# Optimization experiments

Measured on AMD Instinct MI355X. Metric: run time of the kernel, lower is better.

The kernel has to match this reference:

```python
import jax, jax.numpy as jnp
import numpy as np

NUM_CAPS_OUT = 10
NUM_NODES = 32 * 6 * 6  # 1152
IN_DIM = 8
OUT_DIM = 16
ROUTING_ITERS = 3


def squash(x):
    # scale = |x|^2/(1+|x|^2); out = scale * x/|x|  (no epsilon, faithful to torch)
    sn = jnp.sum(x * x, axis=-1, keepdims=True)
    return sn / (1.0 + sn) * x / jnp.sqrt(sn)


def setup_inputs() -> dict:
    key = jax.random.key(0)
    ks = jax.random.split(key, 6)
    B = 512
    images = jax.random.normal(ks[0], (B, 1, 28, 28), dtype=jnp.float32)
    # ConvLayer: Conv2d(1, 256, k=9, s=1) with bias
    conv1_w = jax.random.normal(ks[1], (256, 1, 9, 9), dtype=jnp.float32) * 0.05
    conv1_b = jnp.zeros((256,), dtype=jnp.float32)
    prim_w = jax.random.normal(ks[2], (8 * 32, 256, 9, 9), dtype=jnp.float32) * 0.01
    prim_b = jnp.zeros((8 * 32,), dtype=jnp.float32)
    # DigitCaps weight: torch.randn(10, 1152, 8, 16)
    W = jax.random.normal(ks[3], (NUM_CAPS_OUT, NUM_NODES, IN_DIM, OUT_DIM), dtype=jnp.float32)
    return {"images": images, "conv1_w": conv1_w, "conv1_b": conv1_b,
            "prim_w": prim_w, "prim_b": prim_b, "W": W}


def reference(images, conv1_w, conv1_b, prim_w, prim_b, W):
    B = images.shape[0]
    dn = ('NCHW', 'OIHW', 'NCHW')
    # ConvLayer: 28x28 -> 20x20, 256 channels, ReLU
    x = jax.lax.conv_general_dilated(images, conv1_w, (1, 1), 'VALID', dimension_numbers=dn)
    x = jax.nn.relu(x + conv1_b[None, :, None, None])  # [B,256,20,20]
    # PrimaryCaps: 8 stacked convs -> [B, 8*32, 6, 6]; each capsule viewed as (32*6*6,)
    u = jax.lax.conv_general_dilated(x, prim_w, (2, 2), 'VALID', dimension_numbers=dn)
    u = u + prim_b[None, :, None, None]
    u = u.reshape(B, 8, NUM_NODES).transpose(0, 2, 1)  # [B,1152,8]
    u = squash(u)
    # DigitCaps: u_hat[c,b,n,o] = sum_i u[b,n,i] * W[c,n,i,o]
    u_hat = jnp.einsum('bni,cnio->cbno', u, W)  # [10,B,1152,16]
    # Dynamic routing (3 iterations). b_ij kept as [...,1]: torch replicates it
    # across the 16 out dims identically, so math is unchanged.
    b_ij = jnp.zeros(u_hat.shape[:-1] + (1,), dtype=u_hat.dtype)
    v_j = None
    for it in range(ROUTING_ITERS):
        c_ij = jax.nn.softmax(b_ij, axis=2)            # softmax over nodes
        s_j = jnp.sum(c_ij * u_hat, axis=2, keepdims=True)  # [10,B,1,16]
        v_j = squash(s_j)
        if it < ROUTING_ITERS - 1:
            a_ij = jnp.sum(u_hat * v_j, axis=-1, keepdims=True)  # [10,B,1152,1]
            b_ij = b_ij + a_ij
    # squeeze -> [10,B,16], transpose(0,1) -> [B,10,16]
    return v_j[:, :, 0, :].transpose(1, 0, 2)
```

## Files before the change

### kernel.cpp

```cpp
#include <hip/hip_runtime.h>
#include <hip/hip_bf16.h>
#include <cstddef>
#include <cstdint>

typedef __attribute__((ext_vector_type(8))) short v8s;
typedef __attribute__((ext_vector_type(16))) float v16f;

#define GLDS(SRC, DST) __builtin_amdgcn_global_load_lds( \
    (const __attribute__((address_space(1))) void*)(SRC), \
    (__attribute__((address_space(3))) void*)(DST), 16, 0, 0)

#define WAIT_VM0() asm volatile("s_waitcnt vmcnt(0)" ::: "memory")
#define SCHED0()   __builtin_amdgcn_sched_barrier(0)

__device__ __forceinline__ void bf16split(float x, unsigned short& h, unsigned short& l) {
    union { float f; unsigned u; } a; a.f = x;
    unsigned r = a.u + 0x7fff + ((a.u >> 16) & 1);
    h = (unsigned short)(r >> 16);
    union { unsigned u; float f; } hb; hb.u = (unsigned)h << 16;
    union { float f; unsigned u; } b; b.f = x - hb.f;
    unsigned r2 = b.u + 0x7fff + ((b.u >> 16) & 1);
    l = (unsigned short)(r2 >> 16);
}

__global__ __launch_bounds__(256) void prep_kernel(
    const float* __restrict__ cw, const float* __restrict__ pw,
    float* __restrict__ wT1, char* __restrict__ wpk)
{
    int idx = blockIdx.x * 256 + threadIdx.x;
    if (idx < 81 * 256) {
        int k = idx >> 8, oc = idx & 255;
        wT1[idx] = cw[oc * 81 + k];
    }
    int Q = idx & 2047;
    int slab = idx >> 11;
    int D = Q << 4;
    int R = D >> 9;
    int v = (D & 511) ^ ((R & 31) << 4);
    int h = v >> 7, pl = (v >> 6) & 1, icb = v & 63;
    int ch = h * 64 + R;
    int g = slab / 81, k = slab - g * 81;
    int ic0 = g * 32 + (icb >> 1);
    const float* src = pw + ((size_t)ch * 256 + ic0) * 81 + k;
    v8s ov;
#pragma unroll
    for (int j = 0; j < 8; ++j) {
        unsigned short hh, ll; bf16split(src[(size_t)j * 81], hh, ll);
        ov[j] = (short)(pl ? ll : hh);
    }
    *(v8s*)(wpk + (size_t)slab * 32768 + D) = ov;
}

__global__ __launch_bounds__(256) void conv1_kernel(
    const float* __restrict__ img,
    const float* __restrict__ wT1,
    const float* __restrict__ bias,
    char* __restrict__ xc2,
    int b0)
{
    const int bl = blockIdx.x;
    const int oc = threadIdx.x;
    __shared__ __align__(16) float im[784];
    const float* ib = img + (size_t)(b0 + bl) * 784;
    for (int e = oc; e < 784; e += 256) im[e] = ib[e];
    float w[81];
#pragma unroll
    for (int k = 0; k < 81; ++k) w[k] = wT1[k * 256 + oc];
    float bv = bias[oc];
    __syncthreads();
    char* ob = xc2 + (size_t)bl * 409600;
    for (int oy = 0; oy < 20; ++oy) {
        float a[20];
#pragma unroll
        for (int ox = 0; ox < 20; ++ox) a[ox] = bv;
        for (int ky = 0; ky < 9; ++ky) {
            const float* rp = &im[(oy + ky) * 28];
            float r[28];
#pragma unroll
            for (int q = 0; q < 7; ++q) {
                float4 v4 = *(const float4*)(rp + q * 4);
                r[q * 4] = v4.x; r[q * 4 + 1] = v4.y;
                r[q * 4 + 2] = v4.z; r[q * 4 + 3] = v4.w;
            }
#pragma unroll
            for (int kx = 0; kx < 9; ++kx) {
                float wv = w[ky * 9 + kx];
#pragma unroll
                for (int ox = 0; ox < 20; ++ox)
                    a[ox] = fmaf(wv, r[ox + kx], a[ox]);
            }
        }
#pragma unroll
        for (int ox = 0; ox < 20; ++ox) {
            float av = fmaxf(a[ox], 0.f);
            unsigned short h, l; bf16split(av, h, l);
            char* rp2 = ob + (size_t)(oy * 20 + ox) * 1024;
            *(unsigned short*)(rp2 + oc * 2) = h;
            *(unsigned short*)(rp2 + 512 + oc * 2) = l;
        }
    }
}

__global__ __launch_bounds__(512, 1) void gemm_kernel(
    const char* __restrict__ xc2,
    const char* __restrict__ wpk,
    float* __restrict__ prim,
    int M, int Mtiles, int gm0)
{
    __shared__ __align__(128) char As[2][24576];
    __shared__ __align__(128) char Bs[2][32768];
    const int tid = threadIdx.x;
    const int w = tid >> 6, lane = tid & 63;
    const int wm = w & 1, wn = w >> 1;
    const int col = lane & 31, kg = lane >> 5;
    const int id = blockIdx.x;
    const int g = id / Mtiles;
    const int tile = id - g * Mtiles;
    const int m0 = tile * 192;

    int pbase[3], asrc[3];
#pragma unroll
    for (int i = 0; i < 3; ++i) {
        int d = (w * 3 + i) * 1024 + lane * 16;
        int R = d >> 9;
        int v = (d & 511) ^ ((R & 31) << 4);
        int h = v >> 7, pl = (v >> 6) & 1, icb = v & 63;
        int m = m0 + 48 * h + R; if (m >= M) m = M - 1;
        int b = m / 36, s6 = m - b * 36;
        pbase[i] = b * 400 + (s6 / 6) * 40 + (s6 % 6) * 2;
        asrc[i] = pl * 512 + g * 64 + icb;
    }
    int Abase[3], Ahof[3], Axor[3];
#pragma unroll
    for (int fm = 0; fm < 3; ++fm) {
        int m = wm * 96 + fm * 32 + col;
        int h = m / 48, R = m - h * 48;
        Abase[fm] = R * 512;
        Ahof[fm] = h * 128;
        Axor[fm] = (R & 31) << 4;
    }
    const char* wg = wpk + (size_t)g * 81 * 32768;

    v16f acc[3][2];
#pragma unroll
    for (int i = 0; i < 3; ++i)
#pragma unroll
        for (int j = 0; j < 2; ++j)
#pragma unroll
            for (int e = 0; e < 16; ++e) acc[i][j][e] = 0.f;

    auto gldsA = [&](int nb, int kk, int i) {
        const int koff = (kk / 9) * 20 + (kk % 9);
        GLDS(xc2 + (size_t)(pbase[i] + koff) * 1024 + asrc[i],
             &As[nb][(w * 3 + i) * 1024]);
    };
    auto gldsB = [&](int nb, int kk, int i) {
        const char* bs = wg + (size_t)kk * 32768;
        GLDS(bs + (w * 4 + i) * 1024 + lane * 16,
             &Bs[nb][(w * 4 + i) * 1024]);
    };

#pragma unroll
    for (int i = 0; i < 3; ++i) gldsA(0, 0, i);
#pragma unroll
    for (int i = 0; i < 4; ++i) gldsB(0, 0, i);
    WAIT_VM0(); SCHED0();
    __builtin_amdgcn_s_barrier(); SCHED0();

    const int xr = col << 4;
    for (int k = 0; k < 81; ++k) {
        const int cur = k & 1, nxt = cur ^ 1;
        const bool st = (k < 80);
        const char* Ab = &As[cur][0];
        const char* Bb = &Bs[cur][0];
        v8s Ah[3], Al[3];

#pragma unroll
        for (int p = 0; p < 4; ++p) {
            const int s = p >> 1, fn = p & 1;
            const int vb = s * 32 + kg * 16;
            if (st) {
                if (p == 0) { gldsA(nxt, k + 1, 0); gldsA(nxt, k + 1, 1); }
                else if (p == 1) { gldsA(nxt, k + 1, 2); gldsB(nxt, k + 1, 0); }
                else if (p == 2) { gldsB(nxt, k + 1, 1); gldsB(nxt, k + 1, 2); }
                else { gldsB(nxt, k + 1, 3); }
            }
            if (fn == 0) {
#pragma unroll
                for (int fm = 0; fm < 3; ++fm) {
                    const char* ap = Ab + Abase[fm];
                    Ah[fm] = *(const v8s*)(ap + ((Ahof[fm] + vb) ^ Axor[fm]));
                    Al[fm] = *(const v8s*)(ap + ((Ahof[fm] + 64 + vb) ^ Axor[fm]));
                }
            }
            const char* bp = Bb + (fn * 32 + col) * 512;
            v8s Bh = *(const v8s*)(bp + ((wn * 128 + vb) ^ xr));
            v8s Bl = *(const v8s*)(bp + ((wn * 128 + 64 + vb) ^ xr));

            __builtin_amdgcn_s_barrier();
            SCHED0();
            __builtin_amdgcn_s_setprio(1);
#pragma unroll
            for (int fm = 0; fm < 3; ++fm) {
                acc[fm][fn] = __builtin_amdgcn_mfma_f32_32x32x16_bf16(Al[fm], Bh, acc[fm][fn], 0, 0, 0);
                acc[fm][fn] = __builtin_amdgcn_mfma_f32_32x32x16_bf16(Ah[fm], Bl, acc[fm][fn], 0, 0, 0);
                acc[fm][fn] = __builtin_amdgcn_mfma_f32_32x32x16_bf16(Ah[fm], Bh, acc[fm][fn], 0, 0, 0);
            }
            __builtin_amdgcn_s_setprio(0);
            SCHED0();
            if (p < 3) {
                __builtin_amdgcn_s_barrier();
            } else if (st) {
                WAIT_VM0(); SCHED0();
                __builtin_amdgcn_s_barrier(); SCHED0();
            }
        }
    }

    float* pg = prim + (size_t)gm0 * 256;
#pragma unroll
    for (int fm = 0; fm < 3; ++fm)
#pragma unroll
        for (int fn = 0; fn < 2; ++fn) {
            int ch = wn * 64 + fn * 32 + col;
#pragma unroll
            for (int rg = 0; rg < 16; ++rg) {
                int row = (rg & 3) + 8 * (rg >> 2) + 4 * kg;
                int m = m0 + wm * 96 + fm * 32 + row;
                if (m < M) atomicAdd(&pg[(size_t)m * 256 + ch], acc[fm][fn][rg]);
            }
        }
}

__global__ __launch_bounds__(256) void prim2u_kernel(
    const float* __restrict__ prim, const float* __restrict__ pb,
    float* __restrict__ u, int M)
{
    __shared__ float p[64 * 257];
    __shared__ float bsh[256];
    const int tid = threadIdx.x;
    const int rows0 = blockIdx.x * 64;
    bsh[tid] = pb[tid];
#pragma unroll
    for (int j = 0; j < 16; ++j) {
        int e4 = j * 256 + tid;
        int row = e4 >> 6, c4 = (e4 & 63) << 2;
        int rr = rows0 + row; if (rr >= M) rr = M - 1;
        float4 a = *(const float4*)(prim + (size_t)rr * 256 + c4);
        float* pp = &p[row * 257 + c4];
        pp[0] = a.x; pp[1] = a.y; pp[2] = a.z; pp[3] = a.w;
    }
    __syncthreads();
#pragma unroll
    for (int j = 0; j < 8; ++j) {
        int idx = j * 256 + tid;
        int row = idx & 63, cc = idx >> 6;
        int m = rows0 + row;
        if (m >= M) continue;
        int b = m / 36, s = m - b * 36;
        float p8[8]; float sn = 0.f;
#pragma unroll
        for (int d = 0; d < 8; ++d) {
            float v = p[row * 257 + d * 32 + cc] + bsh[d * 32 + cc];
            p8[d] = v; sn += v * v;
        }
        float fac = sqrtf(sn) / (1.0f + sn);
        float4 o0, o1;
        o0.x = fac * p8[0]; o0.y = fac * p8[1]; o0.z = fac * p8[2]; o0.w = fac * p8[3];
        o1.x = fac * p8[4]; o1.y = fac * p8[5]; o1.z = fac * p8[6]; o1.w = fac * p8[7];
        float* up = u + ((size_t)b * 1152 + cc * 36 + s) * 8;
        *(float4*)up = o0;
        *(float4*)(up + 4) = o1;
    }
}

__global__ __launch_bounds__(512) void routing_kernel(
    const float* __restrict__ u,
    const float* __restrict__ W,
    float* __restrict__ out,
    int B)
{
    const int b0 = blockIdx.x * 2;
    const int c = blockIdx.y;
    const int tid = threadIdx.x;
    __shared__ float uht[2][16][1152];
    __shared__ float bijs[2][1152];
    __shared__ float red[2][4 * 17];
    __shared__ float sred[2][17];
    __shared__ float mred[2][4];

    const float* __restrict__ Wc = W + (size_t)c * (1152 * 128);
    const int b1 = (b0 + 1 < B) ? b0 + 1 : b0;
    const float* __restrict__ ub0 = u + (size_t)b0 * 9216;
    const float* __restrict__ ub1 = u + (size_t)b1 * 9216;

    for (int n = tid; n < 1152; n += 512) {
        const float4* p0 = (const float4*)(ub0 + n * 8);
        const float4* p1 = (const float4*)(ub1 + n * 8);
        float4 a0 = p0[0], a1 = p0[1], c0 = p1[0], c1 = p1[1];
        float uu0[8] = {a0.x, a0.y, a0.z, a0.w, a1.x, a1.y, a1.z, a1.w};
        float uu1[8] = {c0.x, c0.y, c0.z, c0.w, c1.x, c1.y, c1.z, c1.w};
        float acc0[16], acc1[16];
#pragma unroll
        for (int o = 0; o < 16; ++o) { acc0[o] = 0.f; acc1[o] = 0.f; }
        const float* wn = Wc + n * 128;
#pragma unroll
        for (int i = 0; i < 8; ++i)
#pragma unroll
            for (int o = 0; o < 16; ++o) {
                float wv = wn[i * 16 + o];
                acc0[o] = fmaf(uu0[i], wv, acc0[o]);
                acc1[o] = fmaf(uu1[i], wv, acc1[o]);
            }
#pragma unroll
        for (int o = 0; o < 16; ++o) { uht[0][o][n] = acc0[o]; uht[1][o][n] = acc1[o]; }
        bijs[0][n] = 0.f; bijs[1][n] = 0.f;
    }
    __syncthreads();

    const int img = tid >> 8, t = tid & 255;
    const int wid = t >> 6, lane = t & 63;
    const float* __restrict__ UHT = &uht[img][0][0];
    float* __restrict__ bij = bijs[img];
    float* __restrict__ redi = red[img];
    float* __restrict__ sredi = sred[img];
    float* __restrict__ mredi = mred[img];

    float fac = 0.f, inv = 0.f;
    for (int it = 0; it < 3; ++it) {
        float m = -3.4e38f;
        for (int n = t; n < 1152; n += 256) m = fmaxf(m, bij[n]);
#pragma unroll
        for (int off = 32; off > 0; off >>= 1) m = fmaxf(m, __shfl_down(m, off));
        if (lane == 0) mredi[wid] = m;
        __syncthreads();
        float M = fmaxf(fmaxf(mredi[0], mredi[1]), fmaxf(mredi[2], mredi[3]));
        float se = 0.f;
        float sp[16];
#pragma unroll
        for (int o = 0; o < 16; ++o) sp[o] = 0.f;
        for (int n = t; n < 1152; n += 256) {
            float e = expf(bij[n] - M);
            se += e;
#pragma unroll
            for (int o = 0; o < 16; ++o) sp[o] = fmaf(e, UHT[o * 1152 + n], sp[o]);
        }
#pragma unroll
        for (int o = 0; o < 16; ++o)
#pragma unroll
            for (int off = 32; off > 0; off >>= 1) sp[o] += __shfl_down(sp[o], off);
#pragma unroll
        for (int off = 32; off > 0; off >>= 1) se += __shfl_down(se, off);
        if (lane == 0) {
#pragma unroll
            for (int o = 0; o < 16; ++o) redi[wid * 17 + o] = sp[o];
            redi[wid * 17 + 16] = se;
        }
        __syncthreads();
        if (t < 17)
            sredi[t] = redi[t] + redi[17 + t] + redi[34 + t] + redi[51 + t];
        __syncthreads();
        inv = 1.0f / sredi[16];
        float sn = 0.f;
        float sj[16];
#pragma unroll
        for (int o = 0; o < 16; ++o) { sj[o] = sredi[o] * inv; sn = fmaf(sj[o], sj[o], sn); }
        fac = sqrtf(sn) / (1.0f + sn);
        if (it < 2) {
            float v[16];
#pragma unroll
            for (int o = 0; o < 16; ++o) v[o] = fac * sj[o];
            for (int n = t; n < 1152; n += 256) {
                float a = 0.f;
#pragma unroll
                for (int o = 0; o < 16; ++o) a = fmaf(UHT[o * 1152 + n], v[o], a);
                bij[n] += a;
            }
        }
        __syncthreads();
    }
    if (t < 16 && b0 + img < B)
        out[((size_t)(b0 + img) * 10 + c) * 16 + t] = fac * (sredi[t] * inv);
}

extern "C" void kernel_launch(void* const* d_in, const int* in_sizes, int n_in,
                              void* d_out, int out_size, void* d_ws, size_t ws_size,
                              hipStream_t stream) {
    const float* images  = (const float*)d_in[0];
    const float* conv1_w = (const float*)d_in[1];
    const float* conv1_b = (const float*)d_in[2];
    const float* prim_w  = (const float*)d_in[3];
    const float* prim_b  = (const float*)d_in[4];
    const float* W       = (const float*)d_in[5];
    float* out = (float*)d_out;

    const int B = in_sizes[0] / 784;
    const int Mg = B * 36;
    const size_t usz = (size_t)B * 1152 * 8 * 4;
    const size_t xc2_full = (size_t)B * 409600;

    char* wsb = (char*)d_ws;
    size_t off = 0;
    float* wT1 = (float*)(wsb + off);
    off += 81 * 256 * 4;
    off = (off + 1023) & ~(size_t)1023;
    char* wpk = wsb + off;
    off += (size_t)648 * 32768;
    float* prim = (float*)(wsb + off);
    off += (size_t)Mg * 256 * 4;
    size_t rem = (ws_size > off) ? ws_size - off : 0;

    float* u;
    char* xc2base;
    int Bc;
    if (rem >= xc2_full) {
        xc2base = wsb + off;
        u = (float*)xc2base;
        Bc = B;
    } else {
        u = (float*)(wsb + off);
        off += usz;
        rem = (ws_size > off) ? ws_size - off : 0;
        xc2base = wsb + off;
        long Bcmax = (long)(rem / 409600);
        if (Bcmax < 1) Bcmax = 1;
        if (Bcmax > B) Bcmax = B;
        int nch = (int)((B + Bcmax - 1) / Bcmax);
        Bc = (B + nch - 1) / nch;
        Bc = (Bc + 15) & ~15;
        if (Bc > Bcmax) Bc = (int)(Bcmax & ~15L);
        if (Bc < 1) Bc = (int)Bcmax;
    }

    hipMemsetAsync(prim, 0, (size_t)Mg * 256 * 4, stream);
    prep_kernel<<<5184, 256, 0, stream>>>(conv1_w, prim_w, wT1, wpk);

    for (int b0 = 0; b0 < B; b0 += Bc) {
        int bc = (B - b0 < Bc) ? (B - b0) : Bc;
        conv1_kernel<<<bc, 256, 0, stream>>>(images, wT1, conv1_b, xc2base, b0);
        int M = bc * 36;
        int Mtiles = (M + 191) / 192;
        gemm_kernel<<<Mtiles * 8, 512, 0, stream>>>(xc2base, wpk, prim, M, Mtiles, b0 * 36);
    }
    prim2u_kernel<<<(Mg + 63) / 64, 256, 0, stream>>>(prim, prim_b, u, Mg);
    dim3 rg((B + 1) / 2, 10);
    routing_kernel<<<rg, 512, 0, stream>>>(u, W, out, B);
}
```

Measured before the change: 1.190 ms.

## Triple-buffer B tiles two stages ahead in gemm and flatten routing grid

The primary-caps GEMM now keeps three LDS buffers for the weight (B) tiles and prefetches them two k-steps ahead, while A tiles stay double-buffered one step ahead. The end-of-step wait relaxes to vmcnt(4) so the four in-flight B loads can stay outstanding across the barrier. Global-to-LDS issues move after the LDS fragment reads. Separately, the routing kernel uses a 1D grid with the capsule index as the slow dimension, which changes block scheduling order so blocks sharing a capsule's W run together. The cost is an extra 32KB of LDS and reliance on exact vmcnt ordering.

```diff
diff --git a/kernel.cpp b/kernel.cpp
--- a/kernel.cpp
+++ b/kernel.cpp
@@ -10,6 +10,7 @@
     (const __attribute__((address_space(1))) void*)(SRC), \
     (__attribute__((address_space(3))) void*)(DST), 16, 0, 0)
 
+#define WAIT_VM4() asm volatile("s_waitcnt vmcnt(4)" ::: "memory")
 #define WAIT_VM0() asm volatile("s_waitcnt vmcnt(0)" ::: "memory")
 #define SCHED0()   __builtin_amdgcn_sched_barrier(0)
 
@@ -108,7 +109,7 @@
     int M, int Mtiles, int gm0)
 {
     __shared__ __align__(128) char As[2][24576];
-    __shared__ __align__(128) char Bs[2][32768];
+    __shared__ __align__(128) char Bs[3][32768];
     const int tid = threadIdx.x;
     const int w = tid >> 6, lane = tid & 63;
     const int wm = w & 1, wn = w >> 1;
@@ -155,8 +156,7 @@
              &As[nb][(w * 3 + i) * 1024]);
     };
     auto gldsB = [&](int nb, int kk, int i) {
-        const char* bs = wg + (size_t)kk * 32768;
-        GLDS(bs + (w * 4 + i) * 1024 + lane * 16,
+        GLDS(wg + (size_t)kk * 32768 + (w * 4 + i) * 1024 + lane * 16,
              &Bs[nb][(w * 4 + i) * 1024]);
     };
 
@@ -164,27 +164,23 @@
     for (int i = 0; i < 3; ++i) gldsA(0, 0, i);
 #pragma unroll
     for (int i = 0; i < 4; ++i) gldsB(0, 0, i);
-    WAIT_VM0(); SCHED0();
+#pragma unroll
+    for (int i = 0; i < 4; ++i) gldsB(1, 1, i);
+    WAIT_VM4(); SCHED0();
     __builtin_amdgcn_s_barrier(); SCHED0();
 
     const int xr = col << 4;
+    v8s Ah[3], Al[3];
     for (int k = 0; k < 81; ++k) {
-        const int cur = k & 1, nxt = cur ^ 1;
-        const bool st = (k < 80);
-        const char* Ab = &As[cur][0];
-        const char* Bb = &Bs[cur][0];
-        v8s Ah[3], Al[3];
+        const char* Ab = &As[k & 1][0];
+        const char* Bb = &Bs[k % 3][0];
+        const int nA = (k + 1) & 1, nB = (k + 2) % 3;
+        const bool stA = (k < 80), stB = (k < 79);
 
 #pragma unroll
         for (int p = 0; p < 4; ++p) {
             const int s = p >> 1, fn = p & 1;
             const int vb = s * 32 + kg * 16;
-            if (st) {
-                if (p == 0) { gldsA(nxt, k + 1, 0); gldsA(nxt, k + 1, 1); }
-                else if (p == 1) { gldsA(nxt, k + 1, 2); gldsB(nxt, k + 1, 0); }
-                else if (p == 2) { gldsB(nxt, k + 1, 1); gldsB(nxt, k + 1, 2); }
-                else { gldsB(nxt, k + 1, 3); }
-            }
             if (fn == 0) {
 #pragma unroll
                 for (int fm = 0; fm < 3; ++fm) {
@@ -196,6 +192,10 @@
             const char* bp = Bb + (fn * 32 + col) * 512;
             v8s Bh = *(const v8s*)(bp + ((wn * 128 + vb) ^ xr));
             v8s Bl = *(const v8s*)(bp + ((wn * 128 + 64 + vb) ^ xr));
+            if (p == 0) { if (stA) { gldsA(nA, k + 1, 0); gldsA(nA, k + 1, 1); } }
+            else if (p == 1) { if (stA) gldsA(nA, k + 1, 2); if (stB) gldsB(nB, k + 2, 0); }
+            else if (p == 2) { if (stB) { gldsB(nB, k + 2, 1); gldsB(nB, k + 2, 2); } }
+            else { if (stB) gldsB(nB, k + 2, 3); }
 
             __builtin_amdgcn_s_barrier();
             SCHED0();
@@ -210,8 +210,9 @@
             SCHED0();
             if (p < 3) {
                 __builtin_amdgcn_s_barrier();
-            } else if (st) {
-                WAIT_VM0(); SCHED0();
+            } else if (stA) {
+                if (stB) { WAIT_VM4(); } else { WAIT_VM0(); }
+                SCHED0();
                 __builtin_amdgcn_s_barrier(); SCHED0();
             }
         }
@@ -278,10 +279,12 @@
     const float* __restrict__ u,
     const float* __restrict__ W,
     float* __restrict__ out,
-    int B)
+    int B, int npairs)
 {
-    const int b0 = blockIdx.x * 2;
-    const int c = blockIdx.y;
+    const int id = blockIdx.x;
+    const int c = id / npairs;
+    const int pair = id - c * npairs;
+    const int b0 = pair * 2;
     const int tid = threadIdx.x;
     __shared__ float uht[2][16][1152];
     __shared__ float bijs[2][1152];
@@ -443,6 +446,6 @@
         gemm_kernel<<<Mtiles * 8, 512, 0, stream>>>(xc2base, wpk, prim, M, Mtiles, b0 * 36);
     }
     prim2u_kernel<<<(Mg + 63) / 64, 256, 0, stream>>>(prim, prim_b, u, Mg);
-    dim3 rg((B + 1) / 2, 10);
-    routing_kernel<<<rg, 512, 0, stream>>>(u, W, out, B);
-}
+    int npairs = (B + 1) / 2;
+    routing_kernel<<<npairs * 10, 512, 0, stream>>>(u, W, out, B, npairs);
+}
```

Result: faster. 977.2 us (-17.8%).
